# Kernel tuning notes

Measured on AMD Instinct MI355X. Metric: run time of the kernel, lower is better.

Reference implementation:

```python
import jax, jax.numpy as jnp
import numpy as np

ALPHA = 1.0
BETA = 1.0
NUM_BIAS_CLASSES = 2


def setup_inputs() -> dict:
    key = jax.random.key(0)
    k1, k2, k3, k4 = jax.random.split(key, 4)
    N, C, D = 4096, 10, 2048
    logits = jax.random.normal(k1, (N, C), dtype=jnp.float32)
    labels = jax.random.randint(k2, (N,), 0, C)
    biases = jax.random.randint(k3, (N,), 0, NUM_BIAS_CLASSES)
    feats = jax.random.normal(k4, (N, D), dtype=jnp.float32)
    return {"logits": logits, "labels": labels, "biases": biases, "feats": feats}


def reference(logits, labels, biases, feats):
    N = feats.shape[0]
    f32 = jnp.float32

    # ----- cross entropy (mean reduction, matches F.cross_entropy) -----
    logp = jax.nn.log_softmax(logits, axis=-1)
    label_loss = -jnp.mean(jnp.take_along_axis(logp, labels[:, None], axis=1))

    # ----- gram matrix: strict lower triangle of feats @ feats.T, clamped -----
    idx = jnp.arange(N)
    strict_lower = idx[:, None] > idx[None, :]            # [N, N] bool, i > j
    gram = jnp.matmul(feats, feats.T)                     # [N, N]
    gram = jnp.clip(jnp.where(strict_lower, gram, 0.0), -1.0, 1.0)

    # ----- R_ortho: per-bias-class |sum of gram over same-bias strict-lower pairs| -----
    # S_b = sum_{i>j, bias_i=bias_j=b} gram_ij = m_b^T gram m_b  (gram already strict lower)
    B = jax.nn.one_hot(biases, NUM_BIAS_CLASSES, dtype=f32)  # [N, NB]
    S = jnp.einsum('ib,ij,jb->b', B, gram, B)                # [NB]
    counts = jnp.sum(B, axis=0)                              # n_b per bias class
    M = counts * (counts - 1.0) * 0.5                        # strict-lower same-bias pairs
    M_tot_o = jnp.sum(M)
    # if M_b == 0 then S_b == 0, so summing all |S_b| matches the torch loop
    R_ortho = jnp.where(M_tot_o > 0, jnp.sum(jnp.abs(S)) / M_tot_o, 0.0)

    # ----- R_parallel: pairs i>j, same target, bias_i < bias_j (unique() is sorted,
    # so row-bias is the earlier-indexed class and col-bias the later one) -----
    same_target = labels[:, None] == labels[None, :]
    bias_lt = biases[:, None] < biases[None, :]
    pmask = (strict_lower & same_target & bias_lt).astype(f32)
    M_tot_p = jnp.sum(pmask)
    ploss = -0.5 * jnp.sum((1.0 + gram) * pmask)
    R_parallel = jnp.where(M_tot_p > 0, 1.0 + ploss / M_tot_p, 0.0)

    bias_loss = ALPHA * R_ortho + BETA * R_parallel
    return (label_loss, bias_loss)
```

## Files before the change

### kernel.cpp

```cpp
#include <hip/hip_runtime.h>
#include <hip/hip_bf16.h>

typedef short  bf16x8 __attribute__((ext_vector_type(8)));
typedef float  f32x4  __attribute__((ext_vector_type(4)));
typedef unsigned int uint4v __attribute__((ext_vector_type(4)));
typedef unsigned long u64x2 __attribute__((ext_vector_type(2)));
typedef unsigned short ushort_t;

#define GLD_LDS16(gp, lp) __builtin_amdgcn_global_load_lds(                 \
    (const __attribute__((address_space(1))) void*)(gp),                    \
    (__attribute__((address_space(3))) void*)(lp), 16, 0, 0)

static __device__ inline short f2bf(float x) {
    unsigned u = __builtin_bit_cast(unsigned, x);
    u += 0x7fffu + ((u >> 16) & 1u);
    return (short)(u >> 16);
}

__global__ __launch_bounds__(256)
void convert_pair8_kernel(const float* __restrict__ in,
                          unsigned char* __restrict__ out,
                          int N, int D)
{
    int uid = blockIdx.x * blockDim.x + threadIdx.x;
    int nw  = D >> 4;
    if (uid >= N * nw) return;
    int row = uid / nw;
    int w   = uid - row * nw;
    int kt  = w >> 2;
    int g   = (w & 3) ^ ((row >> 1) & 3);
    int k0  = kt * 64 + g * 8;
    const float* s = in + (size_t)row * D + k0;
    f32x4 a0 = *(const f32x4*)s;
    f32x4 a1 = *(const f32x4*)(s + 4);
    f32x4 b0 = *(const f32x4*)(s + 32);
    f32x4 b1 = *(const f32x4*)(s + 36);
    unsigned w0 = __builtin_amdgcn_cvt_pk_fp8_f32(a0[0], a0[1], 0, 0);
    w0 = __builtin_amdgcn_cvt_pk_fp8_f32(a0[2], a0[3], w0, 1);
    unsigned w1 = __builtin_amdgcn_cvt_pk_fp8_f32(a1[0], a1[1], 0, 0);
    w1 = __builtin_amdgcn_cvt_pk_fp8_f32(a1[2], a1[3], w1, 1);
    unsigned w2 = __builtin_amdgcn_cvt_pk_fp8_f32(b0[0], b0[1], 0, 0);
    w2 = __builtin_amdgcn_cvt_pk_fp8_f32(b0[2], b0[3], w2, 1);
    unsigned w3 = __builtin_amdgcn_cvt_pk_fp8_f32(b1[0], b1[1], 0, 0);
    w3 = __builtin_amdgcn_cvt_pk_fp8_f32(b1[2], b1[3], w3, 1);
    uint4v v = {w0, w1, w2, w3};
    *(uint4v*)(out + (size_t)uid * 16) = v;
}

__global__ __launch_bounds__(512, 1)
void gram_p2k64_kernel(const unsigned char* __restrict__ fb,
                       const int* __restrict__ labels,
                       const int* __restrict__ biases,
                       float* __restrict__ accbuf,
                       int N, int D)
{
    __shared__ unsigned char As[3][2][128][64];
    __shared__ unsigned char Bs[3][2][128][64];
    __shared__ int lab_r[256], bia_r[256], lab_c[256], bia_c[256];

    int nt = N >> 8;
    int b  = blockIdx.x;
    int nwg = gridDim.x;
    if ((nwg & 7) == 0) b = (b & 7) * (nwg >> 3) + (b >> 3);
    int r = b / nt, c = b % nt;
    int rowbase = r * 256, colbase = c * 256;

    int tid = threadIdx.x;
    if (tid < 256) {
        lab_r[tid] = labels[rowbase + tid];
        bia_r[tid] = biases[rowbase + tid];
    } else {
        int u = tid - 256;
        lab_c[u] = labels[colbase + u];
        bia_c[u] = biases[colbase + u];
    }

    int lane = tid & 63;
    int wid  = tid >> 6;
    int wr   = wid >> 2;
    int wc   = wid & 3;
    int lrow = lane & 15;
    int kgrp = lane >> 4;

    auto STAGE_A = [&](int slot, int h, int kt) {
        int row = tid >> 2;
        int blk = tid & 3;
        const unsigned char* g =
            fb + (size_t)(rowbase + h * 128 + row) * D + kt * 64 + blk * 16;
        GLD_LDS16(g, &As[slot][h][0][0] + tid * 16);
    };
    auto STAGE_B = [&](int slot, int h, int kt) {
        int row = tid >> 2;
        int blk = tid & 3;
        const unsigned char* g =
            fb + (size_t)(colbase + h * 128 + row) * D + kt * 64 + blk * 16;
        GLD_LDS16(g, &Bs[slot][h][0][0] + tid * 16);
    };

    f32x4 acc[8][4] = {};
    int nkt = D >> 6;

    STAGE_A(0, 0, 0); STAGE_A(0, 1, 0); STAGE_B(0, 0, 0); STAGE_B(0, 1, 0);
    STAGE_A(1, 0, 1); STAGE_A(1, 1, 1); STAGE_B(1, 0, 1); STAGE_B(1, 1, 1);
    asm volatile("s_waitcnt vmcnt(4)" ::: "memory");
    __builtin_amdgcn_s_barrier();

    int hb  = wc >> 1;
    int lcb = (wc & 1) * 64;

    int slot = 0, s2 = 2;
    for (int kt = 0; kt < nkt; ++kt) {
        int stg = (kt + 2 < nkt);
        u64x2 breg[4];

        #pragma unroll
        for (int n = 0; n < 4; ++n) {
            int lc = lcb + n * 16 + lrow;
            int u  = kgrp ^ ((lc >> 1) & 3);
            breg[n] = *(const u64x2*)(&Bs[slot][hb][lc][0] + u * 16);
        }
        u64x2 a0[4];
        #pragma unroll
        for (int mm = 0; mm < 4; ++mm) {
            int lr = mm * 16 + lrow;
            int u  = kgrp ^ ((lr >> 1) & 3);
            a0[mm] = *(const u64x2*)(&As[slot][wr][lr][0] + u * 16);
        }
        if (stg) { STAGE_A(s2, 0, kt + 2); STAGE_A(s2, 1, kt + 2); }
        __builtin_amdgcn_s_barrier();
        asm volatile("s_waitcnt lgkmcnt(0)" ::: "memory");
        __builtin_amdgcn_s_setprio(1);
        #pragma unroll
        for (int mm = 0; mm < 4; ++mm)
            #pragma unroll
            for (int n = 0; n < 4; ++n) {
                acc[mm][n] = __builtin_amdgcn_mfma_f32_16x16x32_fp8_fp8(
                    (long)a0[mm][0], (long)breg[n][0], acc[mm][n], 0, 0, 0);
                acc[mm][n] = __builtin_amdgcn_mfma_f32_16x16x32_fp8_fp8(
                    (long)a0[mm][1], (long)breg[n][1], acc[mm][n], 0, 0, 0);
            }
        __builtin_amdgcn_s_setprio(0);
        __builtin_amdgcn_s_barrier();

        u64x2 a1[4];
        #pragma unroll
        for (int mm = 0; mm < 4; ++mm) {
            int lr = (4 + mm) * 16 + lrow;
            int u  = kgrp ^ ((lr >> 1) & 3);
            a1[mm] = *(const u64x2*)(&As[slot][wr][lr][0] + u * 16);
        }
        if (stg) { STAGE_B(s2, 0, kt + 2); STAGE_B(s2, 1, kt + 2); }
        if (stg)
            asm volatile("s_waitcnt vmcnt(4)" ::: "memory");
        else
            asm volatile("s_waitcnt vmcnt(0)" ::: "memory");
        __builtin_amdgcn_s_barrier();
        asm volatile("s_waitcnt lgkmcnt(0)" ::: "memory");
        __builtin_amdgcn_s_setprio(1);
        #pragma unroll
        for (int mm = 0; mm < 4; ++mm)
            #pragma unroll
            for (int n = 0; n < 4; ++n) {
                acc[4 + mm][n] = __builtin_amdgcn_mfma_f32_16x16x32_fp8_fp8(
                    (long)a1[mm][0], (long)breg[n][0], acc[4 + mm][n], 0, 0, 0);
                acc[4 + mm][n] = __builtin_amdgcn_mfma_f32_16x16x32_fp8_fp8(
                    (long)a1[mm][1], (long)breg[n][1], acc[4 + mm][n], 0, 0, 0);
            }
        __builtin_amdgcn_s_setprio(0);
        __builtin_amdgcn_s_barrier();

        slot = (slot == 2) ? 0 : slot + 1;
        s2   = (s2   == 2) ? 0 : s2 + 1;
    }

    if (r < c) return;

    float s0 = 0.f, s1 = 0.f, ps = 0.f, pc = 0.f;
    #pragma unroll
    for (int m = 0; m < 8; ++m) {
        #pragma unroll
        for (int e = 0; e < 4; ++e) {
            int li = wr * 128 + m * 16 + kgrp * 4 + e;
            int gi = rowbase + li;
            int labi = lab_r[li];
            int bi   = bia_r[li];
            #pragma unroll
            for (int n = 0; n < 4; ++n) {
                int lj = wc * 64 + n * 16 + lrow;
                int gj = colbase + lj;
                if (gi > gj) {
                    float g = acc[m][n][e];
                    g = fminf(fmaxf(g, -1.f), 1.f);
                    int bj = bia_c[lj];
                    if (bi == bj) {
                        if (bi == 0) s0 += g; else s1 += g;
                    } else if (labi == lab_c[lj] && bi < bj) {
                        ps += 1.f + g;
                        pc += 1.f;
                    }
                }
            }
        }
    }
    #pragma unroll
    for (int off = 32; off > 0; off >>= 1) {
        s0 += __shfl_down(s0, off);
        s1 += __shfl_down(s1, off);
        ps += __shfl_down(ps, off);
        pc += __shfl_down(pc, off);
    }
    if (lane == 0) {
        atomicAdd(&accbuf[0], s0);
        atomicAdd(&accbuf[1], s1);
        atomicAdd(&accbuf[2], ps);
        atomicAdd(&accbuf[3], pc);
    }
}

__global__ __launch_bounds__(256, 2)
void gram_fused_kernel(const float* __restrict__ feats,
                       const int* __restrict__ labels,
                       const int* __restrict__ biases,
                       float* __restrict__ accbuf,
                       int N, int D)
{
    __shared__ ushort_t As[128 * 64];
    __shared__ ushort_t Bs[128 * 64];
    __shared__ int lab_r[128], bia_r[128], lab_c[128], bia_c[128];

    int t = blockIdx.x;
    int r = (int)((sqrtf(8.0f * (float)t + 1.0f) - 1.0f) * 0.5f);
    while ((r + 1) * (r + 2) / 2 <= t) ++r;
    while (r * (r + 1) / 2 > t) --r;
    int c = t - r * (r + 1) / 2;
    int rowbase = r * 128, colbase = c * 128;

    int tid = threadIdx.x;
    if (tid < 128) {
        lab_r[tid] = labels[rowbase + tid];
        bia_r[tid] = biases[rowbase + tid];
    } else {
        int u = tid - 128;
        lab_c[u] = labels[colbase + u];
        bia_c[u] = biases[colbase + u];
    }

    int lane = tid & 63;
    int wid  = tid >> 6;
    int wr   = wid >> 1;
    int wc   = wid & 1;
    int lrow = lane & 15;
    int kgrp = lane >> 4;

    f32x4 acc[4][4] = {};

    for (int k0 = 0; k0 < D; k0 += 64) {
        __syncthreads();
        #pragma unroll
        for (int it = 0; it < 4; ++it) {
            int wlin = tid + it * 256;
            int row  = wlin >> 3;
            int kc   = wlin & 7;
            const float* ga = feats + (size_t)(rowbase + row) * D + k0 + kc * 8;
            const float* gb = feats + (size_t)(colbase + row) * D + k0 + kc * 8;
            f32x4 a0 = *(const f32x4*)ga;
            f32x4 a1 = *(const f32x4*)(ga + 4);
            f32x4 b0 = *(const f32x4*)gb;
            f32x4 b1 = *(const f32x4*)(gb + 4);
            bf16x8 av, bv;
            #pragma unroll
            for (int e = 0; e < 4; ++e) {
                av[e]     = f2bf(a0[e]);
                av[e + 4] = f2bf(a1[e]);
                bv[e]     = f2bf(b0[e]);
                bv[e + 4] = f2bf(b1[e]);
            }
            int boff = row * 128 + ((kc * 16) ^ ((row & 7) << 4));
            *(bf16x8*)((char*)As + boff) = av;
            *(bf16x8*)((char*)Bs + boff) = bv;
        }
        __syncthreads();

        #pragma unroll
        for (int kk = 0; kk < 2; ++kk) {
            bf16x8 a[4], bb[4];
            #pragma unroll
            for (int m = 0; m < 4; ++m) {
                int rr = wr * 64 + m * 16 + lrow;
                int off = rr * 128 + ((kk * 64 + kgrp * 16) ^ ((rr & 7) << 4));
                a[m] = *(const bf16x8*)((const char*)As + off);
            }
            #pragma unroll
            for (int n = 0; n < 4; ++n) {
                int cc = wc * 64 + n * 16 + lrow;
                int off = cc * 128 + ((kk * 64 + kgrp * 16) ^ ((cc & 7) << 4));
                bb[n] = *(const bf16x8*)((const char*)Bs + off);
            }
            #pragma unroll
            for (int m = 0; m < 4; ++m)
                #pragma unroll
                for (int n = 0; n < 4; ++n)
                    acc[m][n] = __builtin_amdgcn_mfma_f32_16x16x32_bf16(
                        a[m], bb[n], acc[m][n], 0, 0, 0);
        }
    }

    float s0 = 0.f, s1 = 0.f, ps = 0.f, pc = 0.f;
    #pragma unroll
    for (int m = 0; m < 4; ++m) {
        #pragma unroll
        for (int e = 0; e < 4; ++e) {
            int li = wr * 64 + m * 16 + kgrp * 4 + e;
            int gi = rowbase + li;
            int labi = lab_r[li];
            int bi   = bia_r[li];
            #pragma unroll
            for (int n = 0; n < 4; ++n) {
                int lj = wc * 64 + n * 16 + lrow;
                int gj = colbase + lj;
                if (gi > gj) {
                    float g = acc[m][n][e];
                    g = fminf(fmaxf(g, -1.f), 1.f);
                    int bj = bia_c[lj];
                    if (bi == bj) {
                        if (bi == 0) s0 += g; else s1 += g;
                    } else if (labi == lab_c[lj] && bi < bj) {
                        ps += 1.f + g;
                        pc += 1.f;
                    }
                }
            }
        }
    }
    #pragma unroll
    for (int off = 32; off > 0; off >>= 1) {
        s0 += __shfl_down(s0, off);
        s1 += __shfl_down(s1, off);
        ps += __shfl_down(ps, off);
        pc += __shfl_down(pc, off);
    }
    if (lane == 0) {
        atomicAdd(&accbuf[0], s0);
        atomicAdd(&accbuf[1], s1);
        atomicAdd(&accbuf[2], ps);
        atomicAdd(&accbuf[3], pc);
    }
}

__global__ __launch_bounds__(256)
void ce_count_kernel(const float* __restrict__ logits,
                     const int* __restrict__ labels,
                     const int* __restrict__ biases,
                     float* __restrict__ accbuf,
                     int N, int C)
{
    int i = blockIdx.x * blockDim.x + threadIdx.x;
    float loss = 0.f, c0 = 0.f, c1 = 0.f;
    if (i < N) {
        const float* row = logits + (size_t)i * C;
        float mx = -INFINITY;
        for (int k = 0; k < C; ++k) mx = fmaxf(mx, row[k]);
        float s = 0.f;
        for (int k = 0; k < C; ++k) s += expf(row[k] - mx);
        loss = mx + logf(s) - row[labels[i]];
        if (biases[i] == 0) c0 = 1.f; else c1 = 1.f;
    }
    #pragma unroll
    for (int off = 32; off > 0; off >>= 1) {
        loss += __shfl_down(loss, off);
        c0   += __shfl_down(c0, off);
        c1   += __shfl_down(c1, off);
    }
    if ((threadIdx.x & 63) == 0) {
        atomicAdd(&accbuf[4], loss);
        atomicAdd(&accbuf[5], c0);
        atomicAdd(&accbuf[6], c1);
    }
}

__global__ void finalize_kernel(const float* __restrict__ accbuf,
                                float* __restrict__ out, int N)
{
    float S0 = accbuf[0], S1 = accbuf[1], ps = accbuf[2], pc = accbuf[3];
    float ce = accbuf[4], n0 = accbuf[5], n1 = accbuf[6];
    float Mo = 0.5f * (n0 * (n0 - 1.f) + n1 * (n1 - 1.f));
    float Ro = (Mo > 0.f) ? (fabsf(S0) + fabsf(S1)) / Mo : 0.f;
    float Rp = (pc > 0.f) ? 1.f + (-0.5f * ps) / pc : 0.f;
    out[0] = ce / (float)N;
    out[1] = Ro + Rp;
}

extern "C" void kernel_launch(void* const* d_in, const int* in_sizes, int n_in,
                              void* d_out, int out_size, void* d_ws, size_t ws_size,
                              hipStream_t stream)
{
    const float* logits = (const float*)d_in[0];
    const int*   labels = (const int*)d_in[1];
    const int*   biases = (const int*)d_in[2];
    const float* feats  = (const float*)d_in[3];

    int N = in_sizes[1];
    int C = in_sizes[0] / N;
    int D = in_sizes[3] / N;

    float* accbuf = (float*)d_ws;
    hipMemsetAsync(accbuf, 0, 8 * sizeof(float), stream);

    size_t need = 256 + (size_t)N * D;
    if (ws_size >= need && (N & 255) == 0 && (D & 63) == 0) {
        unsigned char* fb = (unsigned char*)d_ws + 256;
        int nu = N * (D >> 4);
        convert_pair8_kernel<<<(nu + 255) / 256, 256, 0, stream>>>(feats, fb,
                                                                   N, D);
        int nt = N >> 8;
        gram_p2k64_kernel<<<nt * nt, 512, 0, stream>>>(fb, labels, biases,
                                                       accbuf, N, D);
    } else {
        int nt = N / 128;
        int T  = nt * (nt + 1) / 2;
        gram_fused_kernel<<<T, 256, 0, stream>>>(feats, labels, biases, accbuf,
                                                 N, D);
    }
    ce_count_kernel<<<(N + 255) / 256, 256, 0, stream>>>(logits, labels, biases,
                                                         accbuf, N, C);
    finalize_kernel<<<1, 1, 0, stream>>>(accbuf, (float*)d_out, N);
}
```

Before: 134.3 us.

## Add split-K triangular-tile FP8 gram kernel with atomic partial accumulation

Adds a new gram kernel that launches only the lower-triangular 128x128 tiles and splits the K dimension into two halves, doubling the number of workgroups. Each half atomically adds its partial tile into a zeroed global scratch buffer. A per-tile flag counter picks the last-arriving block, which then applies the clamp, bias and label masking and the reductions. This skips the upper-triangle work and raises parallelism, at the cost of a large scratch memset, many global float atomics and extra workspace, and it falls back to the old paths if the workspace is too small.

```diff
diff --git a/kernel.cpp b/kernel.cpp
--- a/kernel.cpp
+++ b/kernel.cpp
@@ -47,6 +47,177 @@
     *(uint4v*)(out + (size_t)uid * 16) = v;
 }
 
+__global__ __launch_bounds__(256, 3)
+void gram_split_kernel(const unsigned char* __restrict__ fb,
+                       const int* __restrict__ labels,
+                       const int* __restrict__ biases,
+                       float* __restrict__ accbuf,
+                       int* __restrict__ flags,
+                       float* __restrict__ P,
+                       int N, int D)
+{
+    __shared__ unsigned char As[3][128][64];
+    __shared__ unsigned char Bs[3][128][64];
+    __shared__ int lab_r[128], bia_r[128], lab_c[128], bia_c[128];
+    __shared__ int oldflag;
+
+    int b = blockIdx.x;
+    int nwg = gridDim.x;
+    if ((nwg & 7) == 0) b = (b & 7) * (nwg >> 3) + (b >> 3);
+    int t = b >> 1;
+    int h = b & 1;
+
+    int r = (int)((sqrtf(8.0f * (float)t + 1.0f) - 1.0f) * 0.5f);
+    while ((r + 1) * (r + 2) / 2 <= t) ++r;
+    while (r * (r + 1) / 2 > t) --r;
+    int c = t - r * (r + 1) / 2;
+    int rowbase = r * 128, colbase = c * 128;
+
+    int tid = threadIdx.x;
+    if (tid < 128) {
+        lab_r[tid] = labels[rowbase + tid];
+        bia_r[tid] = biases[rowbase + tid];
+    } else {
+        int u = tid - 128;
+        lab_c[u] = labels[colbase + u];
+        bia_c[u] = biases[colbase + u];
+    }
+
+    int lane = tid & 63;
+    int wid  = tid >> 6;
+    int wr   = wid >> 1;
+    int wc   = wid & 1;
+    int lrow = lane & 15;
+    int kgrp = lane >> 4;
+
+    int kb  = h * (D >> 1);
+    int nkt = (D >> 1) >> 6;
+
+    auto STAGE_A = [&](int slot, int kt) {
+        #pragma unroll
+        for (int i = 0; i < 2; ++i) {
+            int j   = i * 256 + tid;
+            int row = j >> 2;
+            int blk = j & 3;
+            const unsigned char* g =
+                fb + (size_t)(rowbase + row) * D + kb + kt * 64 + blk * 16;
+            GLD_LDS16(g, &As[slot][0][0] + j * 16);
+        }
+    };
+    auto STAGE_B = [&](int slot, int kt) {
+        #pragma unroll
+        for (int i = 0; i < 2; ++i) {
+            int j   = i * 256 + tid;
+            int row = j >> 2;
+            int blk = j & 3;
+            const unsigned char* g =
+                fb + (size_t)(colbase + row) * D + kb + kt * 64 + blk * 16;
+            GLD_LDS16(g, &Bs[slot][0][0] + j * 16);
+        }
+    };
+
+    f32x4 acc[4][4] = {};
+
+    STAGE_A(0, 0); STAGE_B(0, 0);
+    STAGE_A(1, 1); STAGE_B(1, 1);
+    asm volatile("s_waitcnt vmcnt(4)" ::: "memory");
+    __builtin_amdgcn_s_barrier();
+
+    int slot = 0, s2 = 2;
+    for (int kt = 0; kt < nkt; ++kt) {
+        int stg = (kt + 2 < nkt);
+
+        u64x2 a[4], bfr[4];
+        #pragma unroll
+        for (int m = 0; m < 4; ++m) {
+            int lr = wr * 64 + m * 16 + lrow;
+            int u  = kgrp ^ ((lr >> 1) & 3);
+            a[m] = *(const u64x2*)(&As[slot][lr][0] + u * 16);
+        }
+        #pragma unroll
+        for (int n = 0; n < 4; ++n) {
+            int lc = wc * 64 + n * 16 + lrow;
+            int u  = kgrp ^ ((lc >> 1) & 3);
+            bfr[n] = *(const u64x2*)(&Bs[slot][lc][0] + u * 16);
+        }
+        if (stg) { STAGE_A(s2, kt + 2); STAGE_B(s2, kt + 2); }
+        if (stg)
+            asm volatile("s_waitcnt vmcnt(4)" ::: "memory");
+        else
+            asm volatile("s_waitcnt vmcnt(0)" ::: "memory");
+        __builtin_amdgcn_s_barrier();
+        asm volatile("s_waitcnt lgkmcnt(0)" ::: "memory");
+        __builtin_amdgcn_s_setprio(1);
+        #pragma unroll
+        for (int m = 0; m < 4; ++m)
+            #pragma unroll
+            for (int n = 0; n < 4; ++n) {
+                acc[m][n] = __builtin_amdgcn_mfma_f32_16x16x32_fp8_fp8(
+                    (long)a[m][0], (long)bfr[n][0], acc[m][n], 0, 0, 0);
+                acc[m][n] = __builtin_amdgcn_mfma_f32_16x16x32_fp8_fp8(
+                    (long)a[m][1], (long)bfr[n][1], acc[m][n], 0, 0, 0);
+            }
+        __builtin_amdgcn_s_setprio(0);
+        __builtin_amdgcn_s_barrier();
+
+        slot = (slot == 2) ? 0 : slot + 1;
+        s2   = (s2   == 2) ? 0 : s2 + 1;
+    }
+
+    float* Pt = P + (size_t)t * 16384;
+    #pragma unroll
+    for (int m = 0; m < 4; ++m)
+        #pragma unroll
+        for (int e = 0; e < 4; ++e) {
+            int li = wr * 64 + m * 16 + kgrp * 4 + e;
+            #pragma unroll
+            for (int n = 0; n < 4; ++n) {
+                int lj = wc * 64 + n * 16 + lrow;
+                atomicAdd(&Pt[li * 128 + lj], acc[m][n][e]);
+            }
+        }
+    __syncthreads();
+    __threadfence();
+    if (tid == 0) oldflag = atomicAdd(&flags[t], 1);
+    __syncthreads();
+    if (oldflag != 1) return;
+
+    __threadfence();
+    float s0 = 0.f, s1 = 0.f, ps = 0.f, pc = 0.f;
+    for (int j = 0; j < 64; ++j) {
+        int idx = j * 256 + tid;
+        int li = idx >> 7;
+        int lj = idx & 127;
+        int gi = rowbase + li;
+        int gj = colbase + lj;
+        float g = atomicAdd(&Pt[idx], 0.0f);
+        if (gi > gj) {
+            g = fminf(fmaxf(g, -1.f), 1.f);
+            int bi = bia_r[li];
+            int bj = bia_c[lj];
+            if (bi == bj) {
+                if (bi == 0) s0 += g; else s1 += g;
+            } else if (lab_r[li] == lab_c[lj] && bi < bj) {
+                ps += 1.f + g;
+                pc += 1.f;
+            }
+        }
+    }
+    #pragma unroll
+    for (int off = 32; off > 0; off >>= 1) {
+        s0 += __shfl_down(s0, off);
+        s1 += __shfl_down(s1, off);
+        ps += __shfl_down(ps, off);
+        pc += __shfl_down(pc, off);
+    }
+    if (lane == 0) {
+        atomicAdd(&accbuf[0], s0);
+        atomicAdd(&accbuf[1], s1);
+        atomicAdd(&accbuf[2], ps);
+        atomicAdd(&accbuf[3], pc);
+    }
+}
+
 __global__ __launch_bounds__(512, 1)
 void gram_p2k64_kernel(const unsigned char* __restrict__ fb,
                        const int* __restrict__ labels,
@@ -404,11 +575,28 @@
     int D = in_sizes[3] / N;
 
     float* accbuf = (float*)d_ws;
-    hipMemsetAsync(accbuf, 0, 8 * sizeof(float), stream);
-
-    size_t need = 256 + (size_t)N * D;
-    if (ws_size >= need && (N & 255) == 0 && (D & 63) == 0) {
-        unsigned char* fb = (unsigned char*)d_ws + 256;
+    int*   flags  = (int*)((char*)d_ws + 4096);
+    unsigned char* fb = (unsigned char*)d_ws + 8192;
+
+    int ntt = N / 128;
+    int Tt  = ntt * (ntt + 1) / 2;
+    size_t fbSz  = (size_t)N * D;
+    size_t pOff  = (8192 + fbSz + 255) & ~(size_t)255;
+    size_t pSz   = (size_t)Tt * 16384 * sizeof(float);
+    float* P     = (float*)((char*)d_ws + pOff);
+
+    hipMemsetAsync(d_ws, 0, 8192, stream);
+
+    bool conform = ((N & 127) == 0) && ((D & 127) == 0);
+    if (conform && ws_size >= pOff + pSz) {
+        hipMemsetAsync(P, 0, pSz, stream);
+        int nu = N * (D >> 4);
+        convert_pair8_kernel<<<(nu + 255) / 256, 256, 0, stream>>>(feats, fb,
+                                                                   N, D);
+        gram_split_kernel<<<2 * Tt, 256, 0, stream>>>(fb, labels, biases,
+                                                      accbuf, flags, P, N, D);
+    } else if (((N & 255) == 0) && ((D & 63) == 0) &&
+               ws_size >= 8192 + fbSz) {
         int nu = N * (D >> 4);
         convert_pair8_kernel<<<(nu + 255) / 256, 256, 0, stream>>>(feats, fb,
                                                                    N, D);
@@ -416,10 +604,8 @@
         gram_p2k64_kernel<<<nt * nt, 512, 0, stream>>>(fb, labels, biases,
                                                        accbuf, N, D);
     } else {
-        int nt = N / 128;
-        int T  = nt * (nt + 1) / 2;
-        gram_fused_kernel<<<T, 256, 0, stream>>>(feats, labels, biases, accbuf,
-                                                 N, D);
+        gram_fused_kernel<<<Tt, 256, 0, stream>>>(feats, labels, biases,
+                                                  accbuf, N, D);
     }
     ce_count_kernel<<<(N + 255) / 256, 256, 0, stream>>>(logits, labels, biases,
                                                          accbuf, N, C);
```

After: 294.0 us. +118.8%, slower.
